# Kernel optimization log

Hardware: AMD Instinct MI355X
Metric: run time of the kernel (lower is better)

The kernel has to match this reference:

```python
import jax, jax.numpy as jnp
import numpy as np

B, T = 4, 1024
L, D_IN = 3, 1024          # num HM-LSTM layers, per-layer hidden size
D = L * D_IN               # concatenated hidden size (3072)
EMB = 2048                 # shared embedding size
N_LIN = 2                  # linear_sizes = [2048, 2048]
OUT = 32000                # vocab
SCALE = 0.02


def setup_inputs() -> dict:
    key = jax.random.key(0)
    ks = jax.random.split(key, 8)
    return {
        "x": jax.random.normal(ks[0], (B, T, D), jnp.float32),
        "w": jax.random.normal(ks[1], (L, D), jnp.float32) * SCALE,        # gate weights, one [D] vector per layer
        "emb_w": jax.random.normal(ks[2], (L, D_IN, EMB), jnp.float32) * SCALE,
        "emb_b": jax.random.normal(ks[3], (L, EMB), jnp.float32) * SCALE,
        "lin_w": jax.random.normal(ks[4], (N_LIN, EMB, EMB), jnp.float32) * SCALE,
        "lin_b": jax.random.normal(ks[5], (N_LIN, EMB), jnp.float32) * SCALE,
        "out_w": jax.random.normal(ks[6], (EMB, OUT), jnp.float32) * SCALE,
        "out_b": jax.random.normal(ks[7], (OUT,), jnp.float32) * SCALE,
    }


def reference(x, w, emb_w, emb_b, lin_w, lin_b, out_w, out_b):
    Bx, Tx, Dx = x.shape
    # Per-layer scalar gates: sg_l = h @ w_l, g = sigmoid(sg)  -> [B, T, L]
    g = jax.nn.sigmoid(jnp.einsum('btd,ld->btl', x, w))
    # Split concatenated hidden into layers: [B, T, L, D_IN]
    xl = x.reshape(Bx, Tx, L, D_IN)
    # s = sum_l Linear_l(h_l * g_l); biases sum across layers
    s = jnp.einsum('btl,btli,lie->bte', g, xl, emb_w) + emb_b.sum(axis=0)
    h = jax.nn.relu(s)
    # fnn: stacked linears with tanh activation after each
    for i in range(lin_w.shape[0]):
        h = jnp.tanh(h @ lin_w[i] + lin_b[i])
    # final output projection
    return h @ out_w + out_b
```

## Files before the change

### kernel.cpp

```cpp
#include <hip/hip_runtime.h>
#include <math.h>

typedef __attribute__((ext_vector_type(8))) short short8;
typedef __attribute__((ext_vector_type(8))) unsigned short ushort8;
typedef __attribute__((ext_vector_type(4))) unsigned short ushort4v;
typedef __attribute__((ext_vector_type(4))) unsigned int uint4v;
typedef __attribute__((ext_vector_type(4))) float f32x4;
typedef __attribute__((ext_vector_type(16))) float f32x16;

__device__ __forceinline__ unsigned short f2bf(float f) {
  union { float f; unsigned u; } v; v.f = f;
  unsigned u = v.u;
  return (unsigned short)((u + 0x7fffu + ((u >> 16) & 1u)) >> 16);
}

__device__ __forceinline__ void gload_lds16(const void* g, void* lds) {
  __builtin_amdgcn_global_load_lds(
      (const __attribute__((address_space(1))) unsigned int*)g,
      (__attribute__((address_space(3))) unsigned int*)lds, 16, 0, 0);
}

__global__ __launch_bounds__(256)
void gates_kernel(const float* __restrict__ x, const float* __restrict__ w,
                  unsigned short* __restrict__ xg) {
  const int n = blockIdx.x;
  const int t = threadIdx.x;
  const float* xr = x + (size_t)n * 3072;

  f32x4 xv[3];
#pragma unroll
  for (int c = 0; c < 3; ++c)
    xv[c] = *(const f32x4*)(xr + c * 1024 + t * 4);

  float p[3] = {0.f, 0.f, 0.f};
#pragma unroll
  for (int l = 0; l < 3; ++l) {
#pragma unroll
    for (int c = 0; c < 3; ++c) {
      f32x4 wv = *(const f32x4*)(w + l * 3072 + c * 1024 + t * 4);
      p[l] += xv[c][0] * wv[0] + xv[c][1] * wv[1] + xv[c][2] * wv[2] + xv[c][3] * wv[3];
    }
  }
#pragma unroll
  for (int off = 32; off; off >>= 1) {
    p[0] += __shfl_xor(p[0], off);
    p[1] += __shfl_xor(p[1], off);
    p[2] += __shfl_xor(p[2], off);
  }
  __shared__ float sred[4][3];
  const int wave = t >> 6, lane = t & 63;
  if (lane == 0) {
    sred[wave][0] = p[0]; sred[wave][1] = p[1]; sred[wave][2] = p[2];
  }
  __syncthreads();
  float g[3];
#pragma unroll
  for (int l = 0; l < 3; ++l) {
    float s = sred[0][l] + sred[1][l] + sred[2][l] + sred[3][l];
    g[l] = 1.f / (1.f + expf(-s));
  }
  unsigned short* orow = xg + (size_t)n * 3072;
#pragma unroll
  for (int c = 0; c < 3; ++c) {
    ushort4v o;
#pragma unroll
    for (int j = 0; j < 4; ++j) o[j] = f2bf(xv[c][j] * g[c]);
    *(ushort4v*)(orow + c * 1024 + t * 4) = o;
  }
}

__global__ __launch_bounds__(256)
void transcvt_kernel(const float* __restrict__ in, unsigned short* __restrict__ outp,
                     int R, int C) {
  __shared__ float tile[64][65];
  const int c0 = blockIdx.x * 64, r0 = blockIdx.y * 64;
  const int t = threadIdx.x;
  const int tr = t >> 4;
  const int tc = (t & 15) * 4;
#pragma unroll
  for (int p = 0; p < 4; ++p) {
    int r = p * 16 + tr;
    f32x4 v = *(const f32x4*)(in + (size_t)(r0 + r) * C + c0 + tc);
    tile[r][tc] = v[0]; tile[r][tc + 1] = v[1];
    tile[r][tc + 2] = v[2]; tile[r][tc + 3] = v[3];
  }
  __syncthreads();
  const int c = t >> 2;
  const int rb = (t & 3) * 16;
  ushort8 o0, o1;
#pragma unroll
  for (int j = 0; j < 8; ++j) o0[j] = f2bf(tile[rb + j][c]);
#pragma unroll
  for (int j = 0; j < 8; ++j) o1[j] = f2bf(tile[rb + 8 + j][c]);
  unsigned short* dst = outp + (size_t)(c0 + c) * R + r0 + rb;
  *(ushort8*)dst = o0;
  *(ushort8*)(dst + 8) = o1;
}

template <int EPI>
__global__ __launch_bounds__(256)
void gemm_tt(const unsigned short* __restrict__ A,
             const unsigned short* __restrict__ Bt,
             const float* __restrict__ bias,
             unsigned short* __restrict__ Cb,
             float* __restrict__ Cf,
             int K, int N) {
  __shared__ __align__(16) unsigned short As[128 * 64];
  __shared__ __align__(16) unsigned short Bs[128 * 64];

  const int tid = threadIdx.x;
  const int lane = tid & 63;
  const int wv = tid >> 6;
  const int wm = wv >> 1, wn = wv & 1;
  const int bid = blockIdx.x;
  const int cpx = gridDim.x >> 3;
  const int lid = (bid & 7) * cpx + (bid >> 3);
  const int mt = lid & 31;
  const int nt = lid >> 5;
  const int m0 = mt * 128, n0 = nt * 128;
  const size_t strideB = (size_t)K * 2;

  f32x4 acc[4][4] = {};

  for (int kt = 0; kt < K; kt += 64) {
    __syncthreads();
#pragma unroll
    for (int i = 0; i < 4; ++i) {
      const int o = wv * 4096 + i * 1024 + lane * 16;
      const int row = o >> 7;
      const int sw = (((o >> 4) & 7) * 16) ^ ((row & 7) << 4);
      gload_lds16((const char*)A + (size_t)(m0 + row) * strideB + (size_t)kt * 2 + sw,
                  (char*)As + wv * 4096 + i * 1024);
      gload_lds16((const char*)Bt + (size_t)(n0 + row) * strideB + (size_t)kt * 2 + sw,
                  (char*)Bs + wv * 4096 + i * 1024);
    }
    __syncthreads();
#pragma unroll
    for (int kk = 0; kk < 2; ++kk) {
      short8 av[4], bv[4];
      const int kb = kk * 64 + (lane >> 4) * 16;
#pragma unroll
      for (int mi = 0; mi < 4; ++mi) {
        int row = wm * 64 + mi * 16 + (lane & 15);
        av[mi] = *(const short8*)((const char*)As + row * 128 + (kb ^ ((row & 7) << 4)));
      }
#pragma unroll
      for (int ni = 0; ni < 4; ++ni) {
        int row = wn * 64 + ni * 16 + (lane & 15);
        bv[ni] = *(const short8*)((const char*)Bs + row * 128 + (kb ^ ((row & 7) << 4)));
      }
#pragma unroll
      for (int mi = 0; mi < 4; ++mi)
#pragma unroll
        for (int ni = 0; ni < 4; ++ni)
          acc[mi][ni] = __builtin_amdgcn_mfma_f32_16x16x32_bf16(av[mi], bv[ni], acc[mi][ni], 0, 0, 0);
    }
  }

  const int lr = lane >> 4, lc = lane & 15;
#pragma unroll
  for (int ni = 0; ni < 4; ++ni) {
    int c = n0 + wn * 64 + ni * 16 + lc;
    float bb;
    if (EPI == 0) bb = bias[c] + bias[N + c] + bias[2 * N + c];
    else          bb = bias[c];
#pragma unroll
    for (int mi = 0; mi < 4; ++mi) {
      int r0 = m0 + wm * 64 + mi * 16 + lr * 4;
      f32x4 v = acc[mi][ni];
#pragma unroll
      for (int j = 0; j < 4; ++j) {
        float val = v[j] + bb;
        size_t idx = (size_t)(r0 + j) * N + c;
        if (EPI == 0) { val = val > 0.f ? val : 0.f; Cb[idx] = f2bf(val); }
        else if (EPI == 1) { Cb[idx] = f2bf(tanhf(val)); }
        else { Cf[idx] = val; }
      }
    }
  }
}

__global__ __launch_bounds__(512, 2)
void gemm8_out(const unsigned short* __restrict__ A,
               const unsigned short* __restrict__ Bt,
               const float* __restrict__ bias,
               float* __restrict__ Cf,
               int K, int N) {
  __shared__ __align__(16) unsigned short As8[2][256 * 64];
  __shared__ __align__(16) unsigned short Bs8[2][256 * 64];

  const int tid = threadIdx.x;
  const int lane = tid & 63;
  const int wid = tid >> 6;
  const int wm = wid >> 2, wn = wid & 3;

  const int bid = blockIdx.x;
  const int cpx = gridDim.x >> 3;
  const int lid = (bid & 7) * cpx + (bid >> 3);
  const int mt = lid & 15;
  const int ntile = lid >> 4;
  const int m0 = mt * 256, n0 = ntile * 256;
  const size_t strideB = (size_t)K * 2;
  const int kTiles = K >> 6;

  const unsigned short* smat = (wid < 4) ? A : Bt;
  char* sb = (wid < 4) ? (char*)As8 : (char*)Bs8;
  const int part = wid & 3;
  const int srow0 = ((wid < 4) ? m0 : n0) + part * 64 + (lane >> 3);
  const int ssw = ((lane & 7) ^ (lane >> 3)) << 4;

  auto stage8 = [&](int buf, int t) {
#pragma unroll
    for (int i = 0; i < 8; ++i)
      gload_lds16((const char*)smat + (size_t)(srow0 + i * 8) * strideB +
                      (size_t)t * 128 + ssw,
                  sb + buf * 32768 + part * 8192 + i * 1024);
  };

  const int l31 = lane & 31;
  const int hk16 = (lane >> 5) * 16;

  f32x16 acc[4][2] = {};

  stage8(0, 0);
  stage8(1, 1);
  asm volatile("s_waitcnt vmcnt(8)" ::: "memory");
  __builtin_amdgcn_sched_barrier(0);
  __builtin_amdgcn_s_barrier();

  for (int t = 0; t < kTiles; ++t) {
    const char* ab = (const char*)As8 + (t & 1) * 32768;
    const char* bb = (const char*)Bs8 + (t & 1) * 32768;
    short8 av[2][4], bva[4], bvb[4];

#pragma unroll
    for (int mi = 0; mi < 2; ++mi) {
      int r = wm * 128 + mi * 32 + l31;
      int sz = (r & 7) << 4;
#pragma unroll
      for (int ks = 0; ks < 4; ++ks)
        av[mi][ks] = *(const short8*)(ab + r * 128 + ((ks * 32 + hk16) ^ sz));
    }
    {
      int r = wn * 64 + l31;
      int sz = (r & 7) << 4;
#pragma unroll
      for (int ks = 0; ks < 4; ++ks)
        bva[ks] = *(const short8*)(bb + r * 128 + ((ks * 32 + hk16) ^ sz));
    }
    __builtin_amdgcn_s_setprio(1);
#pragma unroll
    for (int ks = 0; ks < 4; ++ks)
#pragma unroll
      for (int mi = 0; mi < 2; ++mi)
        acc[mi][0] = __builtin_amdgcn_mfma_f32_32x32x16_bf16(
            av[mi][ks], bva[ks], acc[mi][0], 0, 0, 0);
    __builtin_amdgcn_s_setprio(0);

    {
      int r = wn * 64 + 32 + l31;
      int sz = (r & 7) << 4;
#pragma unroll
      for (int ks = 0; ks < 4; ++ks)
        bvb[ks] = *(const short8*)(bb + r * 128 + ((ks * 32 + hk16) ^ sz));
    }
    __builtin_amdgcn_s_setprio(1);
#pragma unroll
    for (int ks = 0; ks < 4; ++ks)
#pragma unroll
      for (int mi = 0; mi < 2; ++mi)
        acc[mi][1] = __builtin_amdgcn_mfma_f32_32x32x16_bf16(
            av[mi][ks], bvb[ks], acc[mi][1], 0, 0, 0);
    __builtin_amdgcn_s_setprio(0);

#pragma unroll
    for (int mi = 0; mi < 2; ++mi) {
      int r = wm * 128 + 64 + mi * 32 + l31;
      int sz = (r & 7) << 4;
#pragma unroll
      for (int ks = 0; ks < 4; ++ks)
        av[mi][ks] = *(const short8*)(ab + r * 128 + ((ks * 32 + hk16) ^ sz));
    }
    __builtin_amdgcn_s_setprio(1);
#pragma unroll
    for (int ks = 0; ks < 4; ++ks)
#pragma unroll
      for (int mi = 0; mi < 2; ++mi)
        acc[2 + mi][1] = __builtin_amdgcn_mfma_f32_32x32x16_bf16(
            av[mi][ks], bvb[ks], acc[2 + mi][1], 0, 0, 0);
    __builtin_amdgcn_s_setprio(0);

    __builtin_amdgcn_s_setprio(1);
#pragma unroll
    for (int ks = 0; ks < 4; ++ks)
#pragma unroll
      for (int mi = 0; mi < 2; ++mi)
        acc[2 + mi][0] = __builtin_amdgcn_mfma_f32_32x32x16_bf16(
            av[mi][ks], bva[ks], acc[2 + mi][0], 0, 0, 0);
    __builtin_amdgcn_s_setprio(0);

    if (t + 1 < kTiles) {
      __builtin_amdgcn_sched_barrier(0);
      __builtin_amdgcn_s_barrier();
      if (t + 2 < kTiles) {
        stage8(t & 1, t + 2);
        asm volatile("s_waitcnt vmcnt(8)" ::: "memory");
      } else {
        asm volatile("s_waitcnt vmcnt(0)" ::: "memory");
      }
      __builtin_amdgcn_sched_barrier(0);
      __builtin_amdgcn_s_barrier();
    }
  }

  const int rbase = m0 + wm * 128 + 4 * (lane >> 5);
#pragma unroll
  for (int ni = 0; ni < 2; ++ni) {
    int c = n0 + wn * 64 + ni * 32 + l31;
    float bb2 = bias[c];
#pragma unroll
    for (int mi = 0; mi < 4; ++mi) {
#pragma unroll
      for (int rg = 0; rg < 16; ++rg) {
        int r = rbase + mi * 32 + (rg & 3) + 8 * (rg >> 2);
        __builtin_nontemporal_store(acc[mi][ni][rg] + bb2,
                                    &Cf[(size_t)r * N + c]);
      }
    }
  }
}

template <int EPI>
__global__ __launch_bounds__(256)
void gemm_bf16(const unsigned short* __restrict__ A,
               const float* __restrict__ B,
               const float* __restrict__ bias,
               unsigned short* __restrict__ Cb,
               float* __restrict__ Cf,
               int K, int N) {
  __shared__ __align__(16) unsigned short As[128 * 64];
  __shared__ __align__(16) unsigned short Bs[128 * 64];

  const int tid = threadIdx.x;
  const int lane = tid & 63;
  const int wv = tid >> 6;
  const int wm = wv >> 1, wn = wv & 1;
  const int mt = blockIdx.x & 31;
  const int nt = blockIdx.x >> 5;
  const int m0 = mt * 128, n0 = nt * 128;

  f32x4 acc[4][4] = {};

  for (int kt = 0; kt < K; kt += 64) {
    __syncthreads();
#pragma unroll
    for (int i = 0; i < 4; ++i) {
      int q = tid + 256 * i;
      int row = q >> 3;
      int kc = q & 7;
      uint4v v = *(const uint4v*)((const char*)A +
                   ((size_t)(m0 + row) * K + kt) * 2 + kc * 16);
      *(uint4v*)((char*)As + row * 128 + ((kc * 16) ^ ((row & 7) << 4))) = v;
    }
#pragma unroll
    for (int gi = 0; gi < 4; ++gi) {
      int q = tid + 256 * gi;
      int nn = q & 127;
      int k8 = q >> 7;
      const float* src = B + (size_t)(kt + k8 * 8) * N + (n0 + nn);
      ushort8 tv;
#pragma unroll
      for (int j = 0; j < 8; ++j) tv[j] = f2bf(src[(size_t)j * N]);
      *(ushort8*)((char*)Bs + nn * 128 + ((k8 * 16) ^ ((nn & 7) << 4))) = tv;
    }
    __syncthreads();
#pragma unroll
    for (int kk = 0; kk < 2; ++kk) {
      short8 av[4], bv[4];
      const int kb = kk * 64 + (lane >> 4) * 16;
#pragma unroll
      for (int mi = 0; mi < 4; ++mi) {
        int row = wm * 64 + mi * 16 + (lane & 15);
        av[mi] = *(const short8*)((const char*)As + row * 128 + (kb ^ ((row & 7) << 4)));
      }
#pragma unroll
      for (int ni = 0; ni < 4; ++ni) {
        int row = wn * 64 + ni * 16 + (lane & 15);
        bv[ni] = *(const short8*)((const char*)Bs + row * 128 + (kb ^ ((row & 7) << 4)));
      }
#pragma unroll
      for (int mi = 0; mi < 4; ++mi)
#pragma unroll
        for (int ni = 0; ni < 4; ++ni)
          acc[mi][ni] = __builtin_amdgcn_mfma_f32_16x16x32_bf16(av[mi], bv[ni], acc[mi][ni], 0, 0, 0);
    }
  }

  const int lr = lane >> 4, lc = lane & 15;
#pragma unroll
  for (int ni = 0; ni < 4; ++ni) {
    int c = n0 + wn * 64 + ni * 16 + lc;
    float bb = bias[c];
#pragma unroll
    for (int mi = 0; mi < 4; ++mi) {
      int r0 = m0 + wm * 64 + mi * 16 + lr * 4;
      f32x4 v = acc[mi][ni];
#pragma unroll
      for (int j = 0; j < 4; ++j) {
        float val = v[j] + bb;
        size_t idx = (size_t)(r0 + j) * N + c;
        if (EPI == 1) { Cb[idx] = f2bf(tanhf(val)); }
        else { Cf[idx] = val; }
      }
    }
  }
}

extern "C" void kernel_launch(void* const* d_in, const int* in_sizes, int n_in,
                              void* d_out, int out_size, void* d_ws, size_t ws_size,
                              hipStream_t stream) {
  const float* x     = (const float*)d_in[0];
  const float* w     = (const float*)d_in[1];
  const float* emb_w = (const float*)d_in[2];
  const float* emb_b = (const float*)d_in[3];
  const float* lin_w = (const float*)d_in[4];
  const float* lin_b = (const float*)d_in[5];
  const float* out_w = (const float*)d_in[6];
  const float* out_b = (const float*)d_in[7];
  float* out = (float*)d_out;

  char* ob = (char*)d_out;
  unsigned short* xg      = (unsigned short*)ob;
  unsigned short* h0      = (unsigned short*)(ob + (((size_t)128) << 20));
  unsigned short* h1      = (unsigned short*)(ob + (((size_t)160) << 20));
  unsigned short* emb_wT  = (unsigned short*)(ob + (((size_t)192) << 20));
  unsigned short* lin_wT0 = (unsigned short*)(ob + (((size_t)208) << 20));
  unsigned short* lin_wT1 = (unsigned short*)(ob + (((size_t)224) << 20));
  unsigned short* h2      = (unsigned short*)d_ws;
  unsigned short* out_wT  = (unsigned short*)((char*)d_ws + (((size_t)32) << 20));
  const bool fast4 = ws_size >= ((((size_t)32) << 20) + (size_t)32000 * 2048 * 2);

  gates_kernel<<<4096, 256, 0, stream>>>(x, w, xg);
  transcvt_kernel<<<dim3(32, 48), 256, 0, stream>>>(emb_w, emb_wT, 3072, 2048);
  transcvt_kernel<<<dim3(32, 32), 256, 0, stream>>>(lin_w, lin_wT0, 2048, 2048);
  transcvt_kernel<<<dim3(32, 32), 256, 0, stream>>>(lin_w + 2048 * 2048, lin_wT1, 2048, 2048);
  if (fast4)
    transcvt_kernel<<<dim3(500, 32), 256, 0, stream>>>(out_w, out_wT, 2048, 32000);

  gemm_tt<0><<<32 * 16, 256, 0, stream>>>(xg, emb_wT, emb_b, h0, nullptr, 3072, 2048);
  gemm_tt<1><<<32 * 16, 256, 0, stream>>>(h0, lin_wT0, lin_b, h1, nullptr, 2048, 2048);
  gemm_tt<1><<<32 * 16, 256, 0, stream>>>(h1, lin_wT1, lin_b + 2048, h2, nullptr, 2048, 2048);
  if (fast4)
    gemm8_out<<<16 * 125, 512, 0, stream>>>(h2, out_wT, out_b, out, 2048, 32000);
  else
    gemm_bf16<2><<<32 * 250, 256, 0, stream>>>(h2, out_w, out_b, nullptr, out, 2048, 32000);
}
```

Measured before the change: 909.1 us.

## Merge gate/transposes into one launch and overlap out_w transpose with first GEMM

```diff
diff --git a/kernel.cpp b/kernel.cpp
--- a/kernel.cpp
+++ b/kernel.cpp
@@ -20,60 +20,11 @@
       (__attribute__((address_space(3))) unsigned int*)lds, 16, 0, 0);
 }
 
-__global__ __launch_bounds__(256)
-void gates_kernel(const float* __restrict__ x, const float* __restrict__ w,
-                  unsigned short* __restrict__ xg) {
-  const int n = blockIdx.x;
-  const int t = threadIdx.x;
-  const float* xr = x + (size_t)n * 3072;
-
-  f32x4 xv[3];
-#pragma unroll
-  for (int c = 0; c < 3; ++c)
-    xv[c] = *(const f32x4*)(xr + c * 1024 + t * 4);
-
-  float p[3] = {0.f, 0.f, 0.f};
-#pragma unroll
-  for (int l = 0; l < 3; ++l) {
-#pragma unroll
-    for (int c = 0; c < 3; ++c) {
-      f32x4 wv = *(const f32x4*)(w + l * 3072 + c * 1024 + t * 4);
-      p[l] += xv[c][0] * wv[0] + xv[c][1] * wv[1] + xv[c][2] * wv[2] + xv[c][3] * wv[3];
-    }
-  }
-#pragma unroll
-  for (int off = 32; off; off >>= 1) {
-    p[0] += __shfl_xor(p[0], off);
-    p[1] += __shfl_xor(p[1], off);
-    p[2] += __shfl_xor(p[2], off);
-  }
-  __shared__ float sred[4][3];
-  const int wave = t >> 6, lane = t & 63;
-  if (lane == 0) {
-    sred[wave][0] = p[0]; sred[wave][1] = p[1]; sred[wave][2] = p[2];
-  }
-  __syncthreads();
-  float g[3];
-#pragma unroll
-  for (int l = 0; l < 3; ++l) {
-    float s = sred[0][l] + sred[1][l] + sred[2][l] + sred[3][l];
-    g[l] = 1.f / (1.f + expf(-s));
-  }
-  unsigned short* orow = xg + (size_t)n * 3072;
-#pragma unroll
-  for (int c = 0; c < 3; ++c) {
-    ushort4v o;
-#pragma unroll
-    for (int j = 0; j < 4; ++j) o[j] = f2bf(xv[c][j] * g[c]);
-    *(ushort4v*)(orow + c * 1024 + t * 4) = o;
-  }
-}
-
-__global__ __launch_bounds__(256)
-void transcvt_kernel(const float* __restrict__ in, unsigned short* __restrict__ outp,
-                     int R, int C) {
-  __shared__ float tile[64][65];
-  const int c0 = blockIdx.x * 64, r0 = blockIdx.y * 64;
+__device__ __forceinline__ void tc_body(const float* __restrict__ in,
+                                        unsigned short* __restrict__ outp,
+                                        int R, int C, int r0, int c0,
+                                        char* smem) {
+  float (*tile)[65] = (float(*)[65])smem;
   const int t = threadIdx.x;
   const int tr = t >> 4;
   const int tc = (t & 15) * 4;
@@ -95,6 +46,163 @@
   unsigned short* dst = outp + (size_t)(c0 + c) * R + r0 + rb;
   *(ushort8*)dst = o0;
   *(ushort8*)(dst + 8) = o1;
+}
+
+__global__ __launch_bounds__(256)
+void gates_or_tc(const float* __restrict__ x, const float* __restrict__ w,
+                 unsigned short* __restrict__ xg,
+                 const float* __restrict__ emb_w, unsigned short* __restrict__ emb_wT,
+                 const float* __restrict__ lin_w,
+                 unsigned short* __restrict__ lin_wT0,
+                 unsigned short* __restrict__ lin_wT1) {
+  __shared__ __align__(16) char smem[64 * 65 * 4];
+  __shared__ float sred[4][3];
+  const int bid = blockIdx.x;
+  const int t = threadIdx.x;
+
+  if (bid >= 4096) {
+    int b2 = bid - 4096;
+    if (b2 < 1536) {
+      tc_body(emb_w, emb_wT, 3072, 2048, (b2 >> 5) * 64, (b2 & 31) * 64, smem);
+    } else {
+      int b3 = b2 - 1536;
+      const float* in = (b3 < 1024) ? lin_w : (lin_w + 2048 * 2048);
+      unsigned short* outp = (b3 < 1024) ? lin_wT0 : lin_wT1;
+      b3 &= 1023;
+      tc_body(in, outp, 2048, 2048, (b3 >> 5) * 64, (b3 & 31) * 64, smem);
+    }
+    return;
+  }
+
+  const int n = bid;
+  const float* xr = x + (size_t)n * 3072;
+  f32x4 xv[3];
+#pragma unroll
+  for (int c = 0; c < 3; ++c)
+    xv[c] = *(const f32x4*)(xr + c * 1024 + t * 4);
+
+  float p[3] = {0.f, 0.f, 0.f};
+#pragma unroll
+  for (int l = 0; l < 3; ++l) {
+#pragma unroll
+    for (int c = 0; c < 3; ++c) {
+      f32x4 wv = *(const f32x4*)(w + l * 3072 + c * 1024 + t * 4);
+      p[l] += xv[c][0] * wv[0] + xv[c][1] * wv[1] + xv[c][2] * wv[2] + xv[c][3] * wv[3];
+    }
+  }
+#pragma unroll
+  for (int off = 32; off; off >>= 1) {
+    p[0] += __shfl_xor(p[0], off);
+    p[1] += __shfl_xor(p[1], off);
+    p[2] += __shfl_xor(p[2], off);
+  }
+  const int wave = t >> 6, lane = t & 63;
+  if (lane == 0) {
+    sred[wave][0] = p[0]; sred[wave][1] = p[1]; sred[wave][2] = p[2];
+  }
+  __syncthreads();
+  float g[3];
+#pragma unroll
+  for (int l = 0; l < 3; ++l) {
+    float s = sred[0][l] + sred[1][l] + sred[2][l] + sred[3][l];
+    g[l] = 1.f / (1.f + expf(-s));
+  }
+  unsigned short* orow = xg + (size_t)n * 3072;
+#pragma unroll
+  for (int c = 0; c < 3; ++c) {
+    ushort4v o;
+#pragma unroll
+    for (int j = 0; j < 4; ++j) o[j] = f2bf(xv[c][j] * g[c]);
+    *(ushort4v*)(orow + c * 1024 + t * 4) = o;
+  }
+}
+
+__global__ __launch_bounds__(256)
+void gemm0_or_tc(const unsigned short* __restrict__ A,
+                 const unsigned short* __restrict__ Bt,
+                 const float* __restrict__ bias,
+                 unsigned short* __restrict__ Cb,
+                 const float* __restrict__ tc_in,
+                 unsigned short* __restrict__ tc_out,
+                 int do_tc) {
+  __shared__ __align__(16) char smem[32768];
+  const int bid = blockIdx.x;
+
+  if (bid >= 512) {
+    int b2 = bid - 512;
+    tc_body(tc_in, tc_out, 2048, 32000, (b2 / 500) * 64, (b2 % 500) * 64, smem);
+    return;
+  }
+  (void)do_tc;
+
+  unsigned short* As = (unsigned short*)smem;
+  unsigned short* Bs = (unsigned short*)(smem + 16384);
+  constexpr int K = 3072, N = 2048;
+
+  const int tid = threadIdx.x;
+  const int lane = tid & 63;
+  const int wv = tid >> 6;
+  const int wm = wv >> 1, wn = wv & 1;
+  const int lid = (bid & 7) * 64 + (bid >> 3);
+  const int mt = lid & 31;
+  const int nt = lid >> 5;
+  const int m0 = mt * 128, n0 = nt * 128;
+  const size_t strideB = (size_t)K * 2;
+
+  f32x4 acc[4][4] = {};
+
+  for (int kt = 0; kt < K; kt += 64) {
+    __syncthreads();
+#pragma unroll
+    for (int i = 0; i < 4; ++i) {
+      const int o = wv * 4096 + i * 1024 + lane * 16;
+      const int row = o >> 7;
+      const int sw = (((o >> 4) & 7) * 16) ^ ((row & 7) << 4);
+      gload_lds16((const char*)A + (size_t)(m0 + row) * strideB + (size_t)kt * 2 + sw,
+                  (char*)As + wv * 4096 + i * 1024);
+      gload_lds16((const char*)Bt + (size_t)(n0 + row) * strideB + (size_t)kt * 2 + sw,
+                  (char*)Bs + wv * 4096 + i * 1024);
+    }
+    __syncthreads();
+#pragma unroll
+    for (int kk = 0; kk < 2; ++kk) {
+      short8 av[4], bv[4];
+      const int kb = kk * 64 + (lane >> 4) * 16;
+#pragma unroll
+      for (int mi = 0; mi < 4; ++mi) {
+        int row = wm * 64 + mi * 16 + (lane & 15);
+        av[mi] = *(const short8*)((const char*)As + row * 128 + (kb ^ ((row & 7) << 4)));
+      }
+#pragma unroll
+      for (int ni = 0; ni < 4; ++ni) {
+        int row = wn * 64 + ni * 16 + (lane & 15);
+        bv[ni] = *(const short8*)((const char*)Bs + row * 128 + (kb ^ ((row & 7) << 4)));
+      }
+#pragma unroll
+      for (int mi = 0; mi < 4; ++mi)
+#pragma unroll
+        for (int ni = 0; ni < 4; ++ni)
+          acc[mi][ni] = __builtin_amdgcn_mfma_f32_16x16x32_bf16(av[mi], bv[ni], acc[mi][ni], 0, 0, 0);
+    }
+  }
+
+  const int lr = lane >> 4, lc = lane & 15;
+#pragma unroll
+  for (int ni = 0; ni < 4; ++ni) {
+    int c = n0 + wn * 64 + ni * 16 + lc;
+    float bb = bias[c] + bias[N + c] + bias[2 * N + c];
+#pragma unroll
+    for (int mi = 0; mi < 4; ++mi) {
+      int r0 = m0 + wm * 64 + mi * 16 + lr * 4;
+      f32x4 v = acc[mi][ni];
+#pragma unroll
+      for (int j = 0; j < 4; ++j) {
+        float val = v[j] + bb;
+        val = val > 0.f ? val : 0.f;
+        Cb[(size_t)(r0 + j) * N + c] = f2bf(val);
+      }
+    }
+  }
 }
 
 template <int EPI>
@@ -440,14 +548,15 @@
   unsigned short* out_wT  = (unsigned short*)((char*)d_ws + (((size_t)32) << 20));
   const bool fast4 = ws_size >= ((((size_t)32) << 20) + (size_t)32000 * 2048 * 2);
 
-  gates_kernel<<<4096, 256, 0, stream>>>(x, w, xg);
-  transcvt_kernel<<<dim3(32, 48), 256, 0, stream>>>(emb_w, emb_wT, 3072, 2048);
-  transcvt_kernel<<<dim3(32, 32), 256, 0, stream>>>(lin_w, lin_wT0, 2048, 2048);
-  transcvt_kernel<<<dim3(32, 32), 256, 0, stream>>>(lin_w + 2048 * 2048, lin_wT1, 2048, 2048);
+  gates_or_tc<<<4096 + 3584, 256, 0, stream>>>(x, w, xg, emb_w, emb_wT,
+                                               lin_w, lin_wT0, lin_wT1);
   if (fast4)
-    transcvt_kernel<<<dim3(500, 32), 256, 0, stream>>>(out_w, out_wT, 2048, 32000);
-
-  gemm_tt<0><<<32 * 16, 256, 0, stream>>>(xg, emb_wT, emb_b, h0, nullptr, 3072, 2048);
+    gemm0_or_tc<<<512 + 16000, 256, 0, stream>>>(xg, emb_wT, emb_b, h0,
+                                                 out_w, out_wT, 1);
+  else
+    gemm0_or_tc<<<512, 256, 0, stream>>>(xg, emb_wT, emb_b, h0,
+                                         out_w, out_wT, 0);
+
   gemm_tt<1><<<32 * 16, 256, 0, stream>>>(h0, lin_wT0, lin_b, h1, nullptr, 2048, 2048);
   gemm_tt<1><<<32 * 16, 256, 0, stream>>>(h1, lin_wT1, lin_b + 2048, h2, nullptr, 2048, 2048);
   if (fast4)
```

Result: faster. 885.6 us (median of 2 runs) (-2.6%).
